# Kernel tuning notes

Measured on AMD Instinct MI355X. Metric: run time of the kernel, lower is better.

Reference implementation:

```python
import jax, jax.numpy as jnp
import numpy as np

# Channel schedule of FPSRefineNet(num_structure_points=64, in_channel=640, out=False):
# 640->512 (ReLU), 512->256 (ReLU), 256->128 (ReLU), 128->64 (ReLU since out=False)
CH = [640, 512, 256, 128, 64]
BN_EPS = 1e-5


def _conv_bn_relu(x, W, b, g, beta, m, v):
    # 1x1 Conv2d over [B,C,K,S] == channel matmul; BN in eval mode (running stats);
    # dropout is identity in eval.
    x = jnp.einsum('oc,bcks->boks', W, x) + b[None, :, None, None]
    inv = g / jnp.sqrt(v + BN_EPS)
    x = x * inv[None, :, None, None] + (beta - m * inv)[None, :, None, None]
    return jax.nn.relu(x)


def setup_inputs() -> dict:
    key = jax.random.key(0)
    ks = jax.random.split(key, 32)
    d = {}
    d['grouped_xyz'] = jax.random.normal(ks[0], (8, 3, 32, 1024), jnp.float32)
    d['grouped_points'] = jax.random.normal(ks[1], (8, 640, 32, 1024), jnp.float32)
    i = 2
    for li, (cin, cout) in enumerate(zip(CH[:-1], CH[1:])):
        d[f'W{li}'] = jax.random.normal(ks[i], (cout, cin), jnp.float32) / np.sqrt(cin).astype(np.float32); i += 1
        d[f'b{li}'] = jnp.zeros((cout,), jnp.float32)
        d[f'g{li}'] = jnp.ones((cout,), jnp.float32)
        d[f'beta{li}'] = jnp.zeros((cout,), jnp.float32)
        d[f'm{li}'] = 0.1 * jax.random.normal(ks[i], (cout,), jnp.float32); i += 1
        d[f'v{li}'] = 1.0 + 0.1 * jax.random.uniform(ks[i], (cout,), jnp.float32); i += 1
    return d


def reference(grouped_xyz, grouped_points,
              W0, b0, g0, beta0, m0, v0,
              W1, b1, g1, beta1, m1, v1,
              W2, b2, g2, beta2, m2, v2,
              W3, b3, g3, beta3, m3, v3):
    params = [(W0, b0, g0, beta0, m0, v0),
              (W1, b1, g1, beta1, m1, v1),
              (W2, b2, g2, beta2, m2, v2),
              (W3, b3, g3, beta3, m3, v3)]
    x = grouped_points  # [B, 640, K, S]
    for (W, b, g, be, m, v) in params:
        x = _conv_bn_relu(x, W, b, g, be, m, v)
    # softmax over K (dim=2)
    p = jax.nn.softmax(x, axis=2)  # [B, D'=64, K, S]
    # fused weighted sum over K: sum_k p[b,d,k,s]*xyz[b,c,k,s] -> [B, C, D', S]
    offset_xyz = jnp.einsum('bdks,bcks->bcds', p, grouped_xyz)
    return offset_xyz
```

## Files before the change

### kernel.cpp

```cpp
#include <hip/hip_runtime.h>

typedef unsigned short u16;
typedef __attribute__((ext_vector_type(8))) short bf16x8;
typedef __attribute__((ext_vector_type(4))) float f32x4;
typedef __attribute__((ext_vector_type(16))) float f32x16;

__device__ __forceinline__ u16 f2bf(float f) {
  union { float f; unsigned u; } x; x.f = f;
  return (u16)((x.u + 0x7FFFu + ((x.u >> 16) & 1u)) >> 16);
}
__device__ __forceinline__ float bf2f(u16 h) {
  union { unsigned u; float f; } x; x.u = ((unsigned)h) << 16; return x.f;
}


__global__ __launch_bounds__(256) void prep_kernel(
    const float* __restrict__ W0, const float* __restrict__ W1,
    const float* __restrict__ W2, const float* __restrict__ W3,
    const float* __restrict__ b0, const float* __restrict__ g0, const float* __restrict__ be0, const float* __restrict__ m0, const float* __restrict__ v0,
    const float* __restrict__ b1, const float* __restrict__ g1, const float* __restrict__ be1, const float* __restrict__ m1, const float* __restrict__ v1,
    const float* __restrict__ b2, const float* __restrict__ g2, const float* __restrict__ be2, const float* __restrict__ m2, const float* __restrict__ v2,
    const float* __restrict__ b3, const float* __restrict__ g3, const float* __restrict__ be3, const float* __restrict__ m3, const float* __restrict__ v3,
    u16* __restrict__ Wb, float* __restrict__ sc, float* __restrict__ sh)
{
  int i = blockIdx.x * 256 + threadIdx.x;
  if (i < 62464) {
    const float* Ws; int CIN, KS, local, dstb; bool f16 = false;
    if (i < 40960)      { local = i;         Ws = W0; CIN = 640; KS = 40; dstb = 0; }
    else if (i < 57344) { local = i - 40960; Ws = W1; CIN = 512; KS = 32; dstb = 327680; }
    else if (i < 61440) { local = i - 57344; Ws = W2; CIN = 256; KS = 16; dstb = 458752; }
    else                { local = i - 61440; Ws = W3; CIN = 128; KS = 4;  dstb = 491520; f16 = true; }
    int lane = local & 63, fi = local >> 6;
    int ks = fi % KS, mt = fi / KS;
    int row, k;
    if (!f16) { row = mt * 32 + (lane & 31); k = ks * 16 + (lane >> 5) * 8; }
    else      { row = mt * 16 + (lane & 15); k = ks * 32 + (lane >> 4) * 8; }
    const float* s = Ws + (size_t)row * CIN + k;
    bf16x8 pk;
    #pragma unroll
    for (int j = 0; j < 8; ++j) pk[j] = (short)f2bf(s[j]);
    *reinterpret_cast<bf16x8*>(Wb + dstb + (size_t)local * 8) = pk;
  }
  if (i < 960) {
    const float *B, *G, *BE, *M, *V; int c;
    if (i < 512)      { c = i;       B = b0; G = g0; BE = be0; M = m0; V = v0; }
    else if (i < 768) { c = i - 512; B = b1; G = g1; BE = be1; M = m1; V = v1; }
    else if (i < 896) { c = i - 768; B = b2; G = g2; BE = be2; M = m2; V = v2; }
    else              { c = i - 896; B = b3; G = g3; BE = be3; M = m3; V = v3; }
    float inv = G[c] / sqrtf(V[c] + 1e-5f);
    sc[i] = inv;
    sh[i] = (B[c] - M[c]) * inv + BE[c];
  }
}

template<int MT, int NT>
__device__ __forceinline__ void store_act32(f32x16 (&acc)[MT][NT],
    const float* __restrict__ sc, const float* __restrict__ sh,
    int mrow0, int ntb, int lane, u16* __restrict__ dst, int rowB)
{
  const int l31 = lane & 31, khalf = lane >> 5;
  #pragma unroll
  for (int mi = 0; mi < MT; ++mi) {
    #pragma unroll
    for (int rq = 0; rq < 4; ++rq) {
      const int ch0 = mrow0 + mi * 32 + rq * 8 + khalf * 4;
      const f32x4 s4 = *reinterpret_cast<const f32x4*>(sc + ch0);
      const f32x4 h4 = *reinterpret_cast<const f32x4*>(sh + ch0);
      #pragma unroll
      for (int nt = 0; nt < NT; ++nt) {
        const int px = (ntb + nt) * 32 + l31;
        float r0 = fmaxf(acc[mi][nt][rq * 4 + 0] * s4[0] + h4[0], 0.f);
        float r1 = fmaxf(acc[mi][nt][rq * 4 + 1] * s4[1] + h4[1], 0.f);
        float r2 = fmaxf(acc[mi][nt][rq * 4 + 2] * s4[2] + h4[2], 0.f);
        float r3 = fmaxf(acc[mi][nt][rq * 4 + 3] * s4[3] + h4[3], 0.f);
        uint2 pk;
        pk.x = (unsigned)f2bf(r0) | ((unsigned)f2bf(r1) << 16);
        pk.y = (unsigned)f2bf(r2) | ((unsigned)f2bf(r3) << 16);
        const unsigned byte = ((unsigned)(px * rowB + ch0 * 2)) ^ ((unsigned)((px & 7) << 4));
        *reinterpret_cast<uint2*>(reinterpret_cast<char*>(dst) + byte) = pk;
      }
    }
  }
}

__device__ __forceinline__ void load64(const float* __restrict__ gbase, int c, int w, float (&v)[8]) {
  const float* s = gbase + (size_t)(c * 64 + w * 8) * 32768u;
  #pragma unroll
  for (int kk = 0; kk < 8; ++kk) v[kk] = s[(size_t)kk * 32768u];
}
__device__ __forceinline__ void write64(float (&v)[8], char* __restrict__ buf, unsigned wb) {
  bf16x8 pk;
  #pragma unroll
  for (int kk = 0; kk < 8; ++kk) pk[kk] = (short)f2bf(v[kk]);
  *reinterpret_cast<bf16x8*>(buf + wb) = pk;
}

#define P0_MFMA(XB, c) { \
  bf16x8 ar[2][2]; \
  ar[0][0] = *reinterpret_cast<const bf16x8*>(A0 + ((c) * 4 + 0) * 512); \
  ar[0][1] = *reinterpret_cast<const bf16x8*>(A1 + ((c) * 4 + 0) * 512); \
  ar[1][0] = *reinterpret_cast<const bf16x8*>(A0 + ((c) * 4 + 1) * 512); \
  ar[1][1] = *reinterpret_cast<const bf16x8*>(A1 + ((c) * 4 + 1) * 512); \
  __builtin_amdgcn_s_setprio(1); \
  _Pragma("unroll") \
  for (int ksl = 0; ksl < 4; ++ksl) { \
    const unsigned base = ((unsigned)(l31 * 128 + ksl * 32 + khalf * 16)) ^ sw; \
    bf16x8 bb0 = *reinterpret_cast<const bf16x8*>((XB) + base); \
    bf16x8 bb1 = *reinterpret_cast<const bf16x8*>((XB) + base + 4096); \
    acc0[0][0] = __builtin_amdgcn_mfma_f32_32x32x16_bf16(ar[ksl & 1][0], bb0, acc0[0][0], 0, 0, 0); \
    acc0[0][1] = __builtin_amdgcn_mfma_f32_32x32x16_bf16(ar[ksl & 1][0], bb1, acc0[0][1], 0, 0, 0); \
    acc0[1][0] = __builtin_amdgcn_mfma_f32_32x32x16_bf16(ar[ksl & 1][1], bb0, acc0[1][0], 0, 0, 0); \
    acc0[1][1] = __builtin_amdgcn_mfma_f32_32x32x16_bf16(ar[ksl & 1][1], bb1, acc0[1][1], 0, 0, 0); \
    if (ksl < 2) { \
      ar[ksl & 1][0] = *reinterpret_cast<const bf16x8*>(A0 + ((c) * 4 + ksl + 2) * 512); \
      ar[ksl & 1][1] = *reinterpret_cast<const bf16x8*>(A1 + ((c) * 4 + ksl + 2) * 512); \
    } \
  } \
  __builtin_amdgcn_s_setprio(0); \
}

__global__ __launch_bounds__(512, 4) void fused4_kernel(
    const float* __restrict__ gp, const u16* __restrict__ Wb,
    const float* __restrict__ sc, const float* __restrict__ sh,
    u16* __restrict__ x3)
{
  __shared__ u16 smem[40960];
  char* XsA = reinterpret_cast<char*>(smem);
  char* XsB = XsA + 8192;
  u16*  Y0s = smem + 8192;

  const int tid  = threadIdx.x;
  const int lane = tid & 63;
  const int w    = tid >> 6;
  const int l31  = lane & 31, khalf = lane >> 5;
  const unsigned sw = (unsigned)((l31 & 7) << 4);

  const int b  = blockIdx.x >> 9;
  const int jt = blockIdx.x & 511;
  const int j0 = jt << 6;

  const float* gbase = gp + (size_t)b * (640u * 32768u) + (unsigned)(j0 + lane);
  const unsigned wbyte = ((unsigned)(lane * 128 + w * 16)) ^ ((unsigned)((lane & 7) << 4));

  const u16* A0 = Wb + (size_t)(2 * w) * (40 * 512) + lane * 8;
  const u16* A1 = A0 + (size_t)(40 * 512);

  float vA[8], vB[8];
  f32x16 acc0[2][2] = {};

  load64(gbase, 0, w, vA);
  write64(vA, XsA, wbyte);
  load64(gbase, 1, w, vB);
  __syncthreads();

  #pragma unroll 1
  for (int c2 = 0; c2 < 5; ++c2) {
    const int ce = 2 * c2;
    {
      if (ce < 8) load64(gbase, ce + 2, w, vA);
      write64(vB, XsB, wbyte);
      P0_MFMA(XsA, ce);
      __syncthreads();
    }
    const int co = 2 * c2 + 1;
    {
      if (co < 8) load64(gbase, co + 2, w, vB);
      if (co < 9) write64(vA, XsA, wbyte);
      P0_MFMA(XsB, co);
      if (co < 9) __syncthreads();
    }
  }
  store_act32<2, 2>(acc0, sc, sh, w * 64, 0, lane, Y0s, 1024);
  __syncthreads();

  {
    f32x16 acc1[1][2] = {};
    const u16* A = Wb + 327680 + (size_t)w * (32 * 512) + lane * 8;
    bf16x8 ar8[8];
    #pragma unroll
    for (int q = 0; q < 8; ++q) ar8[q] = *reinterpret_cast<const bf16x8*>(A + q * 512);
    __builtin_amdgcn_s_setprio(1);
    #pragma unroll
    for (int ks = 0; ks < 32; ++ks) {
      const unsigned kb = (unsigned)(ks * 32 + khalf * 16);
      bf16x8 bb0 = *reinterpret_cast<const bf16x8*>(reinterpret_cast<const char*>(Y0s) + (((unsigned)(l31 * 1024) + kb) ^ sw));
      bf16x8 bb1 = *reinterpret_cast<const bf16x8*>(reinterpret_cast<const char*>(Y0s) + (((unsigned)((l31 + 32) * 1024) + kb) ^ sw));
      acc1[0][0] = __builtin_amdgcn_mfma_f32_32x32x16_bf16(ar8[ks & 7], bb0, acc1[0][0], 0, 0, 0);
      acc1[0][1] = __builtin_amdgcn_mfma_f32_32x32x16_bf16(ar8[ks & 7], bb1, acc1[0][1], 0, 0, 0);
      if (ks < 24) ar8[ks & 7] = *reinterpret_cast<const bf16x8*>(A + (ks + 8) * 512);
    }
    __builtin_amdgcn_s_setprio(0);
    __syncthreads();
    store_act32<1, 2>(acc1, sc + 512, sh + 512, w * 32, 0, lane, Y0s, 512);
    __syncthreads();
  }

  {
    f32x16 acc2[1][1] = {};
    const u16* A = Wb + 458752 + (size_t)(w & 3) * (16 * 512) + lane * 8;
    const int pxb = (w >> 2) * 32;
    bf16x8 ar8[8];
    #pragma unroll
    for (int q = 0; q < 8; ++q) ar8[q] = *reinterpret_cast<const bf16x8*>(A + q * 512);
    __builtin_amdgcn_s_setprio(1);
    #pragma unroll
    for (int ks = 0; ks < 16; ++ks) {
      const unsigned kb = (unsigned)(ks * 32 + khalf * 16);
      bf16x8 bb0 = *reinterpret_cast<const bf16x8*>(reinterpret_cast<const char*>(Y0s) + (((unsigned)((pxb + l31) * 512) + kb) ^ sw));
      acc2[0][0] = __builtin_amdgcn_mfma_f32_32x32x16_bf16(ar8[ks & 7], bb0, acc2[0][0], 0, 0, 0);
      if (ks < 8) ar8[ks & 7] = *reinterpret_cast<const bf16x8*>(A + (ks + 8) * 512);
    }
    __builtin_amdgcn_s_setprio(0);
    store_act32<1, 1>(acc2, sc + 768, sh + 768, (w & 3) * 32, w >> 2, lane, smem, 256);
    __syncthreads();
  }

  {
    const int r16 = lane & 15, g = lane >> 4;
    f32x4 acc3[2] = {};
    const u16* A = Wb + 491520 + (size_t)(w & 3) * (4 * 512) + lane * 8;
    bf16x8 a4[4];
    #pragma unroll
    for (int q = 0; q < 4; ++q) a4[q] = *reinterpret_cast<const bf16x8*>(A + q * 512);
    const int ntb = (w >> 2) * 2;
    __builtin_amdgcn_s_setprio(1);
    #pragma unroll
    for (int ks = 0; ks < 4; ++ks) {
      #pragma unroll
      for (int nt = 0; nt < 2; ++nt) {
        const int px = (ntb + nt) * 16 + r16;
        const unsigned byte = ((unsigned)(px * 256 + ks * 64 + g * 16)) ^ ((unsigned)((px & 7) << 4));
        bf16x8 bb = *reinterpret_cast<const bf16x8*>(reinterpret_cast<const char*>(smem) + byte);
        acc3[nt] = __builtin_amdgcn_mfma_f32_16x16x32_bf16(a4[ks], bb, acc3[nt], 0, 0, 0);
      }
    }
    __builtin_amdgcn_s_setprio(0);
    const int c0 = (w & 3) * 16 + g * 4;
    const f32x4 s4 = *reinterpret_cast<const f32x4*>(sc + 896 + c0);
    const f32x4 h4 = *reinterpret_cast<const f32x4*>(sh + 896 + c0);
    u16* x3b = x3 + ((size_t)b << 21) + j0;
    #pragma unroll
    for (int nt = 0; nt < 2; ++nt) {
      const int n = (ntb + nt) * 16 + r16;
      #pragma unroll
      for (int r = 0; r < 4; ++r) {
        float vv = fmaxf(acc3[nt][r] * s4[r] + h4[r], 0.f);
        x3b[(size_t)(c0 + r) * 32768 + n] = f2bf(vv);
      }
    }
  }
}

__global__ __launch_bounds__(256) void softmax_ws_kernel(
    const u16* __restrict__ x3, const float* __restrict__ xyz,
    float* __restrict__ out)
{
  const int tid = blockIdx.x * 256 + threadIdx.x;
  const int b = tid >> 16;
  const int rem = tid & 65535;
  const int d = rem >> 10;
  const int s = rem & 1023;

  const u16* xp = x3 + ((size_t)(b * 64 + d) << 15) + s;
  float p[32];
  float mx = -1e30f;
  #pragma unroll
  for (int k = 0; k < 32; ++k) { p[k] = bf2f(xp[(size_t)k << 10]); mx = fmaxf(mx, p[k]); }
  float sum = 0.f;
  #pragma unroll
  for (int k = 0; k < 32; ++k) { p[k] = __expf(p[k] - mx); sum += p[k]; }
  const float inv = 1.0f / sum;

  const float* zp = xyz + (size_t)b * (3 * 32768) + s;
  #pragma unroll
  for (int c = 0; c < 3; ++c) {
    float a = 0.f;
    #pragma unroll
    for (int k = 0; k < 32; ++k) a += p[k] * zp[c * 32768 + (k << 10)];
    out[((size_t)((b * 3 + c) * 64 + d) << 10) + s] = a * inv;
  }
}

extern "C" void kernel_launch(void* const* d_in, const int* in_sizes, int n_in,
                              void* d_out, int out_size, void* d_ws, size_t ws_size,
                              hipStream_t stream) {
  const float* xyz = (const float*)d_in[0];
  const float* gp  = (const float*)d_in[1];
  const float* W0 = (const float*)d_in[2];
  const float* W1 = (const float*)d_in[8];
  const float* W2 = (const float*)d_in[14];
  const float* W3 = (const float*)d_in[20];

  char* ws = (char*)d_ws;
  u16*   Wb = (u16*)ws;
  float* sc = (float*)(ws + 999424);
  float* sh = (float*)(ws + 1003264);
  u16*   x3 = (u16*)(ws + 1007104);

  prep_kernel<<<245, 256, 0, stream>>>(
      W0, W1, W2, W3,
      (const float*)d_in[3],  (const float*)d_in[4],  (const float*)d_in[5],  (const float*)d_in[6],  (const float*)d_in[7],
      (const float*)d_in[9],  (const float*)d_in[10], (const float*)d_in[11], (const float*)d_in[12], (const float*)d_in[13],
      (const float*)d_in[15], (const float*)d_in[16], (const float*)d_in[17], (const float*)d_in[18], (const float*)d_in[19],
      (const float*)d_in[21], (const float*)d_in[22], (const float*)d_in[23], (const float*)d_in[24], (const float*)d_in[25],
      Wb, sc, sh);

  fused4_kernel<<<4096, 512, 0, stream>>>(gp, Wb, sc, sh, x3);

  softmax_ws_kernel<<<2048, 256, 0, stream>>>(x3, xyz, (float*)d_out);
}
```

Baseline: 360.3 us.

## Deepen layer-0 input prefetch to three stages and vectorize softmax kernel

Layer 0 of the fused kernel now keeps three register stages of global input loads in flight instead of two, with the loop fully unrolled. The weight fragments for the next chunk are prefetched across chunk boundaries rather than reloaded at the start of each chunk. The aim is to hide more global-load latency behind the MFMA work. The softmax/weighted-sum kernel processes two adjacent positions per thread using 32-bit bf16 pair loads and float2 loads and stores, halving the grid. This raises register pressure under the launch bound of 512 threads with 4 blocks per CU, which could cause spills.

```diff
diff --git a/kernel.cpp b/kernel.cpp
--- a/kernel.cpp
+++ b/kernel.cpp
@@ -96,28 +96,30 @@
 }
 
 #define P0_MFMA(XB, c) { \
-  bf16x8 ar[2][2]; \
-  ar[0][0] = *reinterpret_cast<const bf16x8*>(A0 + ((c) * 4 + 0) * 512); \
-  ar[0][1] = *reinterpret_cast<const bf16x8*>(A1 + ((c) * 4 + 0) * 512); \
-  ar[1][0] = *reinterpret_cast<const bf16x8*>(A0 + ((c) * 4 + 1) * 512); \
-  ar[1][1] = *reinterpret_cast<const bf16x8*>(A1 + ((c) * 4 + 1) * 512); \
   __builtin_amdgcn_s_setprio(1); \
   _Pragma("unroll") \
   for (int ksl = 0; ksl < 4; ++ksl) { \
     const unsigned base = ((unsigned)(l31 * 128 + ksl * 32 + khalf * 16)) ^ sw; \
     bf16x8 bb0 = *reinterpret_cast<const bf16x8*>((XB) + base); \
     bf16x8 bb1 = *reinterpret_cast<const bf16x8*>((XB) + base + 4096); \
-    acc0[0][0] = __builtin_amdgcn_mfma_f32_32x32x16_bf16(ar[ksl & 1][0], bb0, acc0[0][0], 0, 0, 0); \
-    acc0[0][1] = __builtin_amdgcn_mfma_f32_32x32x16_bf16(ar[ksl & 1][0], bb1, acc0[0][1], 0, 0, 0); \
-    acc0[1][0] = __builtin_amdgcn_mfma_f32_32x32x16_bf16(ar[ksl & 1][1], bb0, acc0[1][0], 0, 0, 0); \
-    acc0[1][1] = __builtin_amdgcn_mfma_f32_32x32x16_bf16(ar[ksl & 1][1], bb1, acc0[1][1], 0, 0, 0); \
-    if (ksl < 2) { \
-      ar[ksl & 1][0] = *reinterpret_cast<const bf16x8*>(A0 + ((c) * 4 + ksl + 2) * 512); \
-      ar[ksl & 1][1] = *reinterpret_cast<const bf16x8*>(A1 + ((c) * 4 + ksl + 2) * 512); \
+    acc0[0][0] = __builtin_amdgcn_mfma_f32_32x32x16_bf16(ar0[ksl & 1], bb0, acc0[0][0], 0, 0, 0); \
+    acc0[0][1] = __builtin_amdgcn_mfma_f32_32x32x16_bf16(ar0[ksl & 1], bb1, acc0[0][1], 0, 0, 0); \
+    acc0[1][0] = __builtin_amdgcn_mfma_f32_32x32x16_bf16(ar1[ksl & 1], bb0, acc0[1][0], 0, 0, 0); \
+    acc0[1][1] = __builtin_amdgcn_mfma_f32_32x32x16_bf16(ar1[ksl & 1], bb1, acc0[1][1], 0, 0, 0); \
+    const int g_ = (c) * 4 + ksl + 2; \
+    if (g_ < 40) { \
+      ar0[ksl & 1] = *reinterpret_cast<const bf16x8*>(A0 + g_ * 512); \
+      ar1[ksl & 1] = *reinterpret_cast<const bf16x8*>(A1 + g_ * 512); \
     } \
   } \
   __builtin_amdgcn_s_setprio(0); \
 }
+
+#define P0_STEP(c, SL, SW) { \
+  if ((c) + 3 <= 9) load64(gbase, (c) + 3, w, SL); \
+  write64(SW, ((c) & 1) ? XsA : XsB, wbyte); \
+  P0_MFMA(((c) & 1) ? XsB : XsA, c); \
+  __syncthreads(); }
 
 __global__ __launch_bounds__(512, 4) void fused4_kernel(
     const float* __restrict__ gp, const u16* __restrict__ Wb,
@@ -145,31 +147,31 @@
   const u16* A0 = Wb + (size_t)(2 * w) * (40 * 512) + lane * 8;
   const u16* A1 = A0 + (size_t)(40 * 512);
 
-  float vA[8], vB[8];
+  float vS0[8], vS1[8], vS2[8];
+  bf16x8 ar0[2], ar1[2];
   f32x16 acc0[2][2] = {};
 
-  load64(gbase, 0, w, vA);
-  write64(vA, XsA, wbyte);
-  load64(gbase, 1, w, vB);
+  load64(gbase, 0, w, vS0);
+  load64(gbase, 1, w, vS1);
+  load64(gbase, 2, w, vS2);
+  ar0[0] = *reinterpret_cast<const bf16x8*>(A0 + 0 * 512);
+  ar1[0] = *reinterpret_cast<const bf16x8*>(A1 + 0 * 512);
+  ar0[1] = *reinterpret_cast<const bf16x8*>(A0 + 1 * 512);
+  ar1[1] = *reinterpret_cast<const bf16x8*>(A1 + 1 * 512);
+  write64(vS0, XsA, wbyte);
   __syncthreads();
 
-  #pragma unroll 1
-  for (int c2 = 0; c2 < 5; ++c2) {
-    const int ce = 2 * c2;
-    {
-      if (ce < 8) load64(gbase, ce + 2, w, vA);
-      write64(vB, XsB, wbyte);
-      P0_MFMA(XsA, ce);
-      __syncthreads();
-    }
-    const int co = 2 * c2 + 1;
-    {
-      if (co < 8) load64(gbase, co + 2, w, vB);
-      if (co < 9) write64(vA, XsA, wbyte);
-      P0_MFMA(XsB, co);
-      if (co < 9) __syncthreads();
-    }
-  }
+  P0_STEP(0, vS0, vS1)
+  P0_STEP(1, vS1, vS2)
+  P0_STEP(2, vS2, vS0)
+  P0_STEP(3, vS0, vS1)
+  P0_STEP(4, vS1, vS2)
+  P0_STEP(5, vS2, vS0)
+  P0_STEP(6, vS0, vS1)
+  P0_STEP(7, vS1, vS2)
+  P0_STEP(8, vS2, vS0)
+  P0_MFMA(XsB, 9)
+
   store_act32<2, 2>(acc0, sc, sh, w * 64, 0, lane, Y0s, 1024);
   __syncthreads();
 
@@ -256,28 +258,41 @@
     float* __restrict__ out)
 {
   const int tid = blockIdx.x * 256 + threadIdx.x;
-  const int b = tid >> 16;
-  const int rem = tid & 65535;
-  const int d = rem >> 10;
-  const int s = rem & 1023;
-
-  const u16* xp = x3 + ((size_t)(b * 64 + d) << 15) + s;
-  float p[32];
-  float mx = -1e30f;
-  #pragma unroll
-  for (int k = 0; k < 32; ++k) { p[k] = bf2f(xp[(size_t)k << 10]); mx = fmaxf(mx, p[k]); }
-  float sum = 0.f;
-  #pragma unroll
-  for (int k = 0; k < 32; ++k) { p[k] = __expf(p[k] - mx); sum += p[k]; }
-  const float inv = 1.0f / sum;
-
-  const float* zp = xyz + (size_t)b * (3 * 32768) + s;
+  const int b = tid >> 15;
+  const int rem = tid & 32767;
+  const int d = rem >> 9;
+  const int s0 = (rem & 511) * 2;
+
+  const u16* xp = x3 + ((size_t)(b * 64 + d) << 15) + s0;
+  float pa[32], pb[32];
+  float mxa = -1e30f, mxb = -1e30f;
+  #pragma unroll
+  for (int k = 0; k < 32; ++k) {
+    const unsigned u = *reinterpret_cast<const unsigned*>(xp + ((size_t)k << 10));
+    const float va = bf2f((u16)(u & 0xFFFFu));
+    const float vb = bf2f((u16)(u >> 16));
+    pa[k] = va; pb[k] = vb;
+    mxa = fmaxf(mxa, va); mxb = fmaxf(mxb, vb);
+  }
+  float sa = 0.f, sb = 0.f;
+  #pragma unroll
+  for (int k = 0; k < 32; ++k) {
+    pa[k] = __expf(pa[k] - mxa); sa += pa[k];
+    pb[k] = __expf(pb[k] - mxb); sb += pb[k];
+  }
+  const float inva = 1.0f / sa, invb = 1.0f / sb;
+
+  const float* zp = xyz + (size_t)b * (3 * 32768) + s0;
   #pragma unroll
   for (int c = 0; c < 3; ++c) {
-    float a = 0.f;
-    #pragma unroll
-    for (int k = 0; k < 32; ++k) a += p[k] * zp[c * 32768 + (k << 10)];
-    out[((size_t)((b * 3 + c) * 64 + d) << 10) + s] = a * inv;
+    float ax = 0.f, ay = 0.f;
+    #pragma unroll
+    for (int k = 0; k < 32; ++k) {
+      const float2 z = *reinterpret_cast<const float2*>(zp + c * 32768 + (k << 10));
+      ax += pa[k] * z.x; ay += pb[k] * z.y;
+    }
+    float2 o; o.x = ax * inva; o.y = ay * invb;
+    *reinterpret_cast<float2*>(out + ((size_t)((b * 3 + c) * 64 + d) << 10) + s0) = o;
   }
 }
 
@@ -307,5 +322,5 @@
 
   fused4_kernel<<<4096, 512, 0, stream>>>(gp, Wb, sc, sh, x3);
 
-  softmax_ws_kernel<<<2048, 256, 0, stream>>>(x3, xyz, (float*)d_out);
-}
+  softmax_ws_kernel<<<1024, 256, 0, stream>>>(x3, xyz, (float*)d_out);
+}
```

After: 441.7 us. 1.23x slower.
